# Optimization experiments

Measured on AMD Instinct MI355X. Metric: run time of the kernel, lower is better.

## Reference

```python
import jax, jax.numpy as jnp
import numpy as np


def setup_inputs() -> dict:
    key = jax.random.key(0)
    ks = jax.random.split(key, 10)
    B, C, T, H, W = 8, 128, 8, 32, 32
    Cq = C // 8
    return {
        "x": jax.random.normal(ks[0], (B, C, T, H, W), dtype=jnp.float32),
        "Wq": jax.random.normal(ks[1], (Cq, C), dtype=jnp.float32) * (1.0 / np.sqrt(C)),
        "bq": jax.random.normal(ks[2], (Cq,), dtype=jnp.float32) * 0.02,
        "Wk": jax.random.normal(ks[3], (Cq, C), dtype=jnp.float32) * (1.0 / np.sqrt(C)),
        "bk": jax.random.normal(ks[4], (Cq,), dtype=jnp.float32) * 0.02,
        "Wv": jax.random.normal(ks[5], (C, C), dtype=jnp.float32) * (1.0 / np.sqrt(C)),
        "bv": jax.random.normal(ks[6], (C,), dtype=jnp.float32) * 0.02,
        "gamma_pam": jax.random.normal(ks[7], (1,), dtype=jnp.float32),
        "gamma_cam": jax.random.normal(ks[8], (1,), dtype=jnp.float32),
        "gamma_tim": jax.random.normal(ks[9], (1,), dtype=jnp.float32),
    }


def reference(x, Wq, bq, Wk, bk, Wv, bv, gamma_pam, gamma_cam, gamma_tim):
    B, C, T, H, W = x.shape
    HW = H * W

    # ---- PAM: position attention over HW, feature dim = (C//8)*T ----
    # 1x1x1 Conv3d == per-position channel matmul
    q = jnp.einsum('bcthw,oc->bothw', x, Wq) + bq[None, :, None, None, None]
    k = jnp.einsum('bcthw,oc->bothw', x, Wk) + bk[None, :, None, None, None]
    v = jnp.einsum('bcthw,oc->bothw', x, Wv) + bv[None, :, None, None, None]
    qf = q.reshape(B, -1, HW)   # [B, (C//8)*T, HW]
    kf = k.reshape(B, -1, HW)
    vf = v.reshape(B, -1, HW)   # [B, C*T, HW]
    energy = jnp.einsum('bcn,bcm->bnm', qf, kf)          # [B, HW, HW]
    attn = jax.nn.softmax(energy, axis=-1)
    # out = bmm(v, attn^T)
    pam = jnp.einsum('bcm,bnm->bcn', vf, attn).reshape(B, C, T, H, W)
    pam = gamma_pam * pam + x

    # ---- CAM: channel attention (C x C) with negated-energy softmax ----
    xc = x.reshape(B, C, -1)                              # [B, C, T*HW]
    e = jnp.einsum('bcn,bdn->bcd', xc, xc)                # [B, C, C]
    e = jnp.max(e, axis=-1, keepdims=True) - e
    a = jax.nn.softmax(e, axis=-1)
    cam = jnp.einsum('bcd,bdn->bcn', a, xc).reshape(B, C, T, H, W)
    cam = gamma_cam * cam + x

    # ---- TIM: temporal attention (T x T) with negated-energy softmax ----
    xt = jnp.transpose(x, (0, 2, 1, 3, 4)).reshape(B, T, -1)  # [B, T, C*HW]
    e = jnp.einsum('btn,bsn->bts', xt, xt)                # [B, T, T]
    e = jnp.max(e, axis=-1, keepdims=True) - e
    a = jax.nn.softmax(e, axis=-1)
    tim = jnp.einsum('bts,bsn->btn', a, xt).reshape(B, T, C, H, W)
    tim = jnp.transpose(tim, (0, 2, 1, 3, 4))
    tim = gamma_tim * tim + x

    return pam + cam + tim
```

## Files before the change

kernel.cpp:

```cpp
#include <hip/hip_runtime.h>
#include <cstdint>

typedef unsigned short u16;
typedef __attribute__((ext_vector_type(8))) short bf16x8;
typedef __attribute__((ext_vector_type(4))) float f32x4;

constexpr int B_  = 8;
constexpr int C_  = 128;
constexpr int CQ  = 16;
constexpr int T_  = 8;
constexpr int HW_ = 1024;
constexpr int P_  = T_ * HW_;
constexpr int F_  = CQ * T_;
constexpr int CT_ = C_ * T_;

static __device__ __forceinline__ u16 f2bf(float f) {
    union { float f; unsigned u; } v; v.f = f;
    unsigned r = v.u + 0x7fffu + ((v.u >> 16) & 1u);
    return (u16)(r >> 16);
}

#define GLOAD16(src, dst)                                                     \
    __builtin_amdgcn_global_load_lds(                                         \
        (const __attribute__((address_space(1))) void*)(src),                 \
        (__attribute__((address_space(3))) void*)(dst), 16, 0, 0)

__global__ __launch_bounds__(256)
void k_qkv(const float* __restrict__ x,
           const float* __restrict__ Wq, const float* __restrict__ bq,
           const float* __restrict__ Wk, const float* __restrict__ bk,
           const float* __restrict__ Wv, const float* __restrict__ bv,
           u16* __restrict__ qt, u16* __restrict__ kt, u16* __restrict__ v16)
{
    __shared__ float xs[128][64];
    const int b   = blockIdx.y;
    const int p0  = blockIdx.x * 64;
    const int t   = p0 >> 10;
    const int hw0 = p0 & 1023;
    const int tid = threadIdx.x;

    #pragma unroll
    for (int r = 0; r < 8; r++) {
        int idx = r * 256 + tid;
        int c   = idx >> 4;
        int pj  = (idx & 15) << 2;
        *(float4*)&xs[c][pj] =
            *(const float4*)&x[((size_t)(b * C_ + c)) * P_ + p0 + pj];
    }
    __syncthreads();

    const int pq = (tid & 15) << 2;
    const int g  = tid >> 4;

    const float* wrow[10];
    float4       acc[10];
    #pragma unroll
    for (int j = 0; j < 10; j++) {
        int oc = g * 10 + j;
        float bias;
        if (oc < 16)      { wrow[j] = Wq + oc * C_;        bias = bq[oc]; }
        else if (oc < 32) { wrow[j] = Wk + (oc - 16) * C_; bias = bk[oc - 16]; }
        else              { wrow[j] = Wv + (oc - 32) * C_; bias = bv[oc - 32]; }
        acc[j] = make_float4(bias, bias, bias, bias);
    }

    for (int c4 = 0; c4 < 32; c4++) {
        float4 xv0 = *(float4*)&xs[c4 * 4 + 0][pq];
        float4 xv1 = *(float4*)&xs[c4 * 4 + 1][pq];
        float4 xv2 = *(float4*)&xs[c4 * 4 + 2][pq];
        float4 xv3 = *(float4*)&xs[c4 * 4 + 3][pq];
        #pragma unroll
        for (int j = 0; j < 10; j++) {
            float4 w = *(const float4*)&wrow[j][c4 * 4];
            acc[j].x += w.x * xv0.x + w.y * xv1.x + w.z * xv2.x + w.w * xv3.x;
            acc[j].y += w.x * xv0.y + w.y * xv1.y + w.z * xv2.y + w.w * xv3.y;
            acc[j].z += w.x * xv0.z + w.y * xv1.z + w.z * xv2.z + w.w * xv3.z;
            acc[j].w += w.x * xv0.w + w.y * xv1.w + w.z * xv2.w + w.w * xv3.w;
        }
    }

    #pragma unroll
    for (int j = 0; j < 10; j++) {
        int oc = g * 10 + j;
        float a4[4] = {acc[j].x, acc[j].y, acc[j].z, acc[j].w};
        if (oc < 16) {
            #pragma unroll
            for (int i = 0; i < 4; i++)
                qt[((size_t)b * HW_ + hw0 + pq + i) * F_ + oc * 8 + t] = f2bf(a4[i]);
        } else if (oc < 32) {
            #pragma unroll
            for (int i = 0; i < 4; i++)
                kt[((size_t)b * HW_ + hw0 + pq + i) * F_ + (oc - 16) * 8 + t] = f2bf(a4[i]);
        } else {
            ushort4 pk;
            pk.x = f2bf(a4[0]); pk.y = f2bf(a4[1]);
            pk.z = f2bf(a4[2]); pk.w = f2bf(a4[3]);
            *(ushort4*)&v16[((size_t)(b * C_ + oc - 32)) * P_ + p0 + pq] = pk;
        }
    }
}

__global__ __launch_bounds__(256)
void k_energy(const u16* __restrict__ qt, const u16* __restrict__ kt,
              float* __restrict__ E)
{
    __shared__ char As[32768];
    __shared__ char Bs[32768];
    const int b  = blockIdx.z;
    const int n0 = blockIdx.y * 128, m0 = blockIdx.x * 128;
    const int tid = threadIdx.x, lane = tid & 63, w = tid >> 6;
    const u16* qb = qt + (size_t)b * HW_ * F_;
    const u16* kb = kt + (size_t)b * HW_ * F_;

    #pragma unroll
    for (int i = 0; i < 8; i++) {
        int c    = w * 8 + i;
        int row  = c * 4 + (lane >> 4);
        int col  = ((lane & 15) ^ (row & 7)) * 8;
        GLOAD16(qb + (size_t)(n0 + row) * F_ + col, As + c * 1024);
        GLOAD16(kb + (size_t)(m0 + row) * F_ + col, Bs + c * 1024);
    }
    __syncthreads();

    const int wr = w >> 1, wc = w & 1;
    f32x4 acc[4][4];
    #pragma unroll
    for (int mi = 0; mi < 4; mi++)
        #pragma unroll
        for (int ni = 0; ni < 4; ni++) acc[mi][ni] = (f32x4){0.f, 0.f, 0.f, 0.f};

    #pragma unroll
    for (int ks = 0; ks < 4; ks++) {
        bf16x8 af[4], bg[4];
        #pragma unroll
        for (int mi = 0; mi < 4; mi++) {
            int row  = wr * 64 + mi * 16 + (lane & 15);
            int slot = (ks * 4 + (lane >> 4)) ^ (row & 7);
            af[mi] = *(const bf16x8*)(As + row * 256 + slot * 16);
            int rb  = wc * 64 + mi * 16 + (lane & 15);
            int sb  = (ks * 4 + (lane >> 4)) ^ (rb & 7);
            bg[mi] = *(const bf16x8*)(Bs + rb * 256 + sb * 16);
        }
        #pragma unroll
        for (int mi = 0; mi < 4; mi++)
            #pragma unroll
            for (int ni = 0; ni < 4; ni++)
                acc[mi][ni] = __builtin_amdgcn_mfma_f32_16x16x32_bf16(
                    af[mi], bg[ni], acc[mi][ni], 0, 0, 0);
    }

    float* Eb = E + (size_t)b * HW_ * HW_;
    #pragma unroll
    for (int mi = 0; mi < 4; mi++)
        #pragma unroll
        for (int ni = 0; ni < 4; ni++)
            #pragma unroll
            for (int r = 0; r < 4; r++)
                Eb[(size_t)(n0 + wr * 64 + mi * 16 + (lane >> 4) * 4 + r) * HW_
                   + m0 + wc * 64 + ni * 16 + (lane & 15)] = acc[mi][ni][r];
}

__global__ __launch_bounds__(256)
void k_softmax(const float* __restrict__ E, u16* __restrict__ A16)
{
    const float* e = E + (size_t)blockIdx.x * HW_;
    const int tid = threadIdx.x;
    float4 v = ((const float4*)e)[tid];
    float m = fmaxf(fmaxf(v.x, v.y), fmaxf(v.z, v.w));
    #pragma unroll
    for (int off = 32; off; off >>= 1) m = fmaxf(m, __shfl_xor(m, off));
    __shared__ float s1[4], s2[4];
    if ((tid & 63) == 0) s1[tid >> 6] = m;
    __syncthreads();
    m = fmaxf(fmaxf(s1[0], s1[1]), fmaxf(s1[2], s1[3]));
    v.x = __expf(v.x - m); v.y = __expf(v.y - m);
    v.z = __expf(v.z - m); v.w = __expf(v.w - m);
    float s = v.x + v.y + v.z + v.w;
    #pragma unroll
    for (int off = 32; off; off >>= 1) s += __shfl_xor(s, off);
    if ((tid & 63) == 0) s2[tid >> 6] = s;
    __syncthreads();
    s = s2[0] + s2[1] + s2[2] + s2[3];
    float inv = 1.0f / s;
    ushort4 pk;
    pk.x = f2bf(v.x * inv); pk.y = f2bf(v.y * inv);
    pk.z = f2bf(v.z * inv); pk.w = f2bf(v.w * inv);
    ((ushort4*)(A16 + (size_t)blockIdx.x * HW_))[tid] = pk;
}

__global__ __launch_bounds__(256)
void k_pv(const u16* __restrict__ v16, const u16* __restrict__ A16,
          const float* __restrict__ gamma_pam, float* __restrict__ out)
{
    __shared__ char As[16384];
    __shared__ char Bs[16384];
    const int b   = blockIdx.z;
    const int ct0 = blockIdx.y * 128, n0 = blockIdx.x * 128;
    const int tid = threadIdx.x, lane = tid & 63, w = tid >> 6;
    const u16* vb = v16 + (size_t)b * CT_ * HW_;
    const u16* ab = A16 + (size_t)b * HW_ * HW_;

    const int wr = w >> 1, wc = w & 1;
    f32x4 acc[4][4];
    #pragma unroll
    for (int mi = 0; mi < 4; mi++)
        #pragma unroll
        for (int ni = 0; ni < 4; ni++) acc[mi][ni] = (f32x4){0.f, 0.f, 0.f, 0.f};

    for (int mc = 0; mc < 1024; mc += 64) {
        #pragma unroll
        for (int i = 0; i < 4; i++) {
            int c   = w * 4 + i;
            int row = c * 8 + (lane >> 3);
            int col = ((lane & 7) ^ (row & 7)) * 8;
            GLOAD16(vb + (size_t)(ct0 + row) * HW_ + mc + col, As + c * 1024);
            GLOAD16(ab + (size_t)(n0  + row) * HW_ + mc + col, Bs + c * 1024);
        }
        __syncthreads();
        #pragma unroll
        for (int ks = 0; ks < 2; ks++) {
            bf16x8 af[4], bg[4];
            #pragma unroll
            for (int mi = 0; mi < 4; mi++) {
                int row  = wr * 64 + mi * 16 + (lane & 15);
                int slot = (ks * 4 + (lane >> 4)) ^ (row & 7);
                af[mi] = *(const bf16x8*)(As + row * 128 + slot * 16);
                int rb  = wc * 64 + mi * 16 + (lane & 15);
                int sb  = (ks * 4 + (lane >> 4)) ^ (rb & 7);
                bg[mi] = *(const bf16x8*)(Bs + rb * 128 + sb * 16);
            }
            #pragma unroll
            for (int mi = 0; mi < 4; mi++)
                #pragma unroll
                for (int ni = 0; ni < 4; ni++)
                    acc[mi][ni] = __builtin_amdgcn_mfma_f32_16x16x32_bf16(
                        af[mi], bg[ni], acc[mi][ni], 0, 0, 0);
        }
        __syncthreads();
    }

    const float gp = gamma_pam[0];
    float* ob = out + (size_t)b * CT_ * HW_;
    #pragma unroll
    for (int mi = 0; mi < 4; mi++)
        #pragma unroll
        for (int ni = 0; ni < 4; ni++)
            #pragma unroll
            for (int r = 0; r < 4; r++)
                ob[(size_t)(ct0 + wr * 64 + mi * 16 + (lane >> 4) * 4 + r) * HW_
                   + n0 + wc * 64 + ni * 16 + (lane & 15)] = gp * acc[mi][ni][r];
}

__global__ __launch_bounds__(256)
void k_cam_partial(const float* __restrict__ x, float* __restrict__ part)
{
    __shared__ float xs[64][132];
    const int b = blockIdx.y, ch = blockIdx.x;
    const int tid = threadIdx.x;
    const int n0 = ch * 256;
    const float* xb = x + (size_t)b * C_ * P_;
    const int tc = (tid & 15) << 3, td = (tid >> 4) << 3;
    float acc[8][8] = {};

    for (int sp = 0; sp < 4; sp++) {
        #pragma unroll
        for (int r = 0; r < 8; r++) {
            int idx = r * 256 + tid;
            int c = idx >> 4, nj = (idx & 15) << 2;
            float4 xv = *(const float4*)&xb[(size_t)c * P_ + n0 + sp * 64 + nj];
            xs[nj + 0][c] = xv.x; xs[nj + 1][c] = xv.y;
            xs[nj + 2][c] = xv.z; xs[nj + 3][c] = xv.w;
        }
        __syncthreads();
        for (int n = 0; n < 64; n++) {
            float4 a0 = *(float4*)&xs[n][tc], a1 = *(float4*)&xs[n][tc + 4];
            float4 b0 = *(float4*)&xs[n][td], b1 = *(float4*)&xs[n][td + 4];
            float av[8] = {a0.x, a0.y, a0.z, a0.w, a1.x, a1.y, a1.z, a1.w};
            float bv[8] = {b0.x, b0.y, b0.z, b0.w, b1.x, b1.y, b1.z, b1.w};
            #pragma unroll
            for (int i = 0; i < 8; i++)
                #pragma unroll
                for (int j = 0; j < 8; j++)
                    acc[i][j] += av[i] * bv[j];
        }
        __syncthreads();
    }
    float* pb = part + ((size_t)(b * 32 + ch)) * C_ * C_;
    #pragma unroll
    for (int i = 0; i < 8; i++) {
        *(float4*)&pb[(size_t)(tc + i) * C_ + td] =
            make_float4(acc[i][0], acc[i][1], acc[i][2], acc[i][3]);
        *(float4*)&pb[(size_t)(tc + i) * C_ + td + 4] =
            make_float4(acc[i][4], acc[i][5], acc[i][6], acc[i][7]);
    }
}

__global__ __launch_bounds__(128)
void k_cam_reduce(const float* __restrict__ part,
                  const float* __restrict__ gamma_cam, u16* __restrict__ acam16)
{
    const int b = blockIdx.y, c = blockIdx.x;
    const int d = threadIdx.x;
    float s = 0.f;
    for (int ch = 0; ch < 32; ch++)
        s += part[(((size_t)(b * 32 + ch)) * C_ + c) * C_ + d];
    float mn = s;
    #pragma unroll
    for (int off = 32; off; off >>= 1) mn = fminf(mn, __shfl_xor(mn, off));
    __shared__ float m1[2], m2[2];
    if ((d & 63) == 0) m1[d >> 6] = mn;
    __syncthreads();
    mn = fminf(m1[0], m1[1]);
    float p = __expf(mn - s);
    float sum = p;
    #pragma unroll
    for (int off = 32; off; off >>= 1) sum += __shfl_xor(sum, off);
    if ((d & 63) == 0) m2[d >> 6] = sum;
    __syncthreads();
    sum = m2[0] + m2[1];
    acam16[((size_t)(b * C_ + c)) * C_ + d] = f2bf(gamma_cam[0] * p / sum);
}

__global__ __launch_bounds__(256)
void k_tim_gram(const float* __restrict__ x, float* __restrict__ e_t)
{
    const int b = blockIdx.y, c = blockIdx.x;
    const int tid = threadIdx.x;
    const float* xb = x + ((size_t)(b * C_ + c)) * P_;
    float acc[8][8] = {};
    for (int r = 0; r < 4; r++) {
        int hw = r * 256 + tid;
        float xv[8];
        #pragma unroll
        for (int t = 0; t < 8; t++) xv[t] = xb[t * HW_ + hw];
        #pragma unroll
        for (int t = 0; t < 8; t++)
            #pragma unroll
            for (int s2 = 0; s2 < 8; s2++)
                acc[t][s2] += xv[t] * xv[s2];
    }
    __shared__ float sm[4][64];
    const int lane = tid & 63, wid = tid >> 6;
    #pragma unroll
    for (int u = 0; u < 64; u++) {
        float vv = acc[u >> 3][u & 7];
        #pragma unroll
        for (int off = 32; off; off >>= 1) vv += __shfl_xor(vv, off);
        if (lane == 0) sm[wid][u] = vv;
    }
    __syncthreads();
    if (tid < 64) {
        float vv = sm[0][tid] + sm[1][tid] + sm[2][tid] + sm[3][tid];
        atomicAdd(&e_t[b * 64 + tid], vv);
    }
}

__global__ __launch_bounds__(512)
void k_tim_softmax(const float* __restrict__ e_t, float* __restrict__ a_t)
{
    const int tid = threadIdx.x;
    float v = e_t[tid];
    float mn = v;
    #pragma unroll
    for (int off = 4; off; off >>= 1) mn = fminf(mn, __shfl_xor(mn, off, 8));
    float p = __expf(mn - v);
    float s = p;
    #pragma unroll
    for (int off = 4; off; off >>= 1) s += __shfl_xor(s, off, 8);
    a_t[tid] = p / s;
}

__global__ __launch_bounds__(256)
void k_xprime(const float* __restrict__ x, const float* __restrict__ atim,
              const float* __restrict__ gamma_tim, float* __restrict__ Xp)
{
    const int b = blockIdx.y, c = blockIdx.x;
    const size_t base = ((size_t)(b * C_ + c)) * P_;
    const int tid = threadIdx.x;
    const float gt = gamma_tim[0];

    float4 xv[8];
    #pragma unroll
    for (int t = 0; t < 8; t++)
        xv[t] = *(const float4*)&x[base + t * HW_ + tid * 4];

    #pragma unroll
    for (int t = 0; t < 8; t++) {
        float4 o = make_float4(3.f * xv[t].x, 3.f * xv[t].y,
                               3.f * xv[t].z, 3.f * xv[t].w);
        #pragma unroll
        for (int s = 0; s < 8; s++) {
            float w = gt * atim[b * 64 + t * 8 + s];
            o.x += w * xv[s].x; o.y += w * xv[s].y;
            o.z += w * xv[s].z; o.w += w * xv[s].w;
        }
        *(float4*)&Xp[base + t * HW_ + tid * 4] = o;
    }
}

__global__ __launch_bounds__(256)
void k_xt(const float* __restrict__ x, u16* __restrict__ xT)
{
    __shared__ char sy[32768];
    const int b  = blockIdx.y;
    const int p0 = blockIdx.x * 128;
    const int tid = threadIdx.x;

    #pragma unroll
    for (int r = 0; r < 16; r++) {
        int lin = r * 256 + tid;
        int c = lin >> 5, j4 = (lin & 31) << 2;
        float4 xv = *(const float4*)&x[((size_t)(b * C_ + c)) * P_ + p0 + j4];
        float a4[4] = {xv.x, xv.y, xv.z, xv.w};
        #pragma unroll
        for (int u = 0; u < 4; u++) {
            int pi = j4 + u;
            int byte = pi * 256 + ((c * 2) ^ (((pi >> 2) & 15) << 4));
            *(u16*)(sy + byte) = f2bf(a4[u]);
        }
    }
    __syncthreads();
    #pragma unroll
    for (int r = 0; r < 8; r++) {
        int lin = r * 256 + tid;
        int pi = lin >> 4, ci8 = (lin & 15) << 3;
        bf16x8 v = *(const bf16x8*)(sy + pi * 256 +
                                    ((ci8 * 2) ^ (((pi >> 2) & 15) << 4)));
        *(bf16x8*)&xT[((size_t)(b * P_ + p0 + pi)) * C_ + ci8] = v;
    }
}

__global__ __launch_bounds__(256)
void k_cam_av(const u16* __restrict__ acam16, const u16* __restrict__ xT,
              const float* __restrict__ Xp, float* __restrict__ out)
{
    const int b  = blockIdx.y;
    const int p0 = blockIdx.x * 128;
    const int tid = threadIdx.x, lane = tid & 63, w = tid >> 6;

    const u16* Ab = acam16 + (size_t)b * C_ * C_;
    const u16* Bb = xT + ((size_t)(b * P_ + p0 + w * 32)) * C_;

    f32x4 acc[8][2];
    #pragma unroll
    for (int mi = 0; mi < 8; mi++) {
        acc[mi][0] = (f32x4){0.f, 0.f, 0.f, 0.f};
        acc[mi][1] = (f32x4){0.f, 0.f, 0.f, 0.f};
    }

    bf16x8 bg[4][2];
    #pragma unroll
    for (int ks = 0; ks < 4; ks++)
        #pragma unroll
        for (int ni = 0; ni < 2; ni++)
            bg[ks][ni] = *(const bf16x8*)(Bb +
                (size_t)(ni * 16 + (lane & 15)) * C_ + ks * 32 + (lane >> 4) * 8);

    #pragma unroll
    for (int mi = 0; mi < 8; mi++) {
        #pragma unroll
        for (int ks = 0; ks < 4; ks++) {
            bf16x8 af = *(const bf16x8*)(Ab +
                (size_t)(mi * 16 + (lane & 15)) * C_ + ks * 32 + (lane >> 4) * 8);
            acc[mi][0] = __builtin_amdgcn_mfma_f32_16x16x32_bf16(
                af, bg[ks][0], acc[mi][0], 0, 0, 0);
            acc[mi][1] = __builtin_amdgcn_mfma_f32_16x16x32_bf16(
                af, bg[ks][1], acc[mi][1], 0, 0, 0);
        }
    }

    float* ob = out + (size_t)b * C_ * P_;
    const float* xp = Xp + (size_t)b * C_ * P_;
    #pragma unroll
    for (int mi = 0; mi < 8; mi++)
        #pragma unroll
        for (int ni = 0; ni < 2; ni++)
            #pragma unroll
            for (int r = 0; r < 4; r++) {
                int c = mi * 16 + (lane >> 4) * 4 + r;
                int p = p0 + w * 32 + ni * 16 + (lane & 15);
                size_t i = (size_t)c * P_ + p;
                ob[i] += acc[mi][ni][r] + xp[i];
            }
}

extern "C" void kernel_launch(void* const* d_in, const int* in_sizes, int n_in,
                              void* d_out, int out_size, void* d_ws, size_t ws_size,
                              hipStream_t stream)
{
    (void)in_sizes; (void)n_in; (void)out_size; (void)ws_size;
    const float* x  = (const float*)d_in[0];
    const float* Wq = (const float*)d_in[1];
    const float* bq = (const float*)d_in[2];
    const float* Wk = (const float*)d_in[3];
    const float* bk = (const float*)d_in[4];
    const float* Wv = (const float*)d_in[5];
    const float* bv = (const float*)d_in[6];
    const float* gp = (const float*)d_in[7];
    const float* gc = (const float*)d_in[8];
    const float* gt = (const float*)d_in[9];
    float* out = (float*)d_out;
    char*  ws  = (char*)d_ws;

    u16*   qtb    = (u16*)(ws + 0);
    u16*   ktb    = (u16*)(ws + (2u << 20));
    u16*   v16    = (u16*)(ws + (4u << 20));
    float* part   = (float*)(ws + (4u << 20));
    float* Ebuf   = (float*)(ws + (20u << 20));
    float* Xp     = (float*)(ws + (20u << 20));
    u16*   A16    = (u16*)(ws + (52u << 20));
    u16*   xT     = (u16*)(ws + (52u << 20));
    u16*   acam16 = (u16*)(ws + (68u << 20));
    float* etim   = (float*)(ws + (68u << 20) + 32768);
    float* atim   = etim + 512;

    hipMemsetAsync(etim, 0, 512 * sizeof(float), stream);

    k_qkv        <<<dim3(128, 8),  256, 0, stream>>>(x, Wq, bq, Wk, bk, Wv, bv,
                                                     qtb, ktb, v16);
    k_energy     <<<dim3(8, 8, 8), 256, 0, stream>>>(qtb, ktb, Ebuf);
    k_softmax    <<<dim3(8192),    256, 0, stream>>>(Ebuf, A16);
    k_tim_gram   <<<dim3(128, 8),  256, 0, stream>>>(x, etim);
    k_tim_softmax<<<dim3(1),       512, 0, stream>>>(etim, atim);
    k_pv         <<<dim3(8, 8, 8), 256, 0, stream>>>(v16, A16, gp, out);
    k_xprime     <<<dim3(128, 8),  256, 0, stream>>>(x, atim, gt, Xp);
    k_xt         <<<dim3(64, 8),   256, 0, stream>>>(x, xT);
    k_cam_partial<<<dim3(32, 8),   256, 0, stream>>>(x, part);
    k_cam_reduce <<<dim3(128, 8),  128, 0, stream>>>(part, gc, acam16);
    k_cam_av     <<<dim3(64, 8),   256, 0, stream>>>(acam16, xT, Xp, out);
}
```

Baseline: 322.6 us.

## Move QKV projection and CAM gram onto bf16 MFMA, store Xp in bf16

The QKV 1x1 conv now runs on MFMA. It takes a bf16 transposed copy of x produced up front by k_prep (which replaces k_xt) and bf16-cast weights from a new cast kernel. The CAM gram matrix, formerly an fp32 FMA outer-product kernel, is computed with a split bf16 hi/lo scheme (three MFMAs per tile) to keep near-fp32 accuracy. The temporal-mixed Xp intermediate is stored as bf16 to halve its traffic. These changes add extra kernels and split buffers that cost memory traffic, and they lower the precision of the projections and of Xp.

```diff
diff --git a/kernel.cpp b/kernel.cpp
--- a/kernel.cpp
+++ b/kernel.cpp
@@ -7,11 +7,10 @@
 
 constexpr int B_  = 8;
 constexpr int C_  = 128;
-constexpr int CQ  = 16;
 constexpr int T_  = 8;
 constexpr int HW_ = 1024;
 constexpr int P_  = T_ * HW_;
-constexpr int F_  = CQ * T_;
+constexpr int F_  = 128;
 constexpr int CT_ = C_ * T_;
 
 static __device__ __forceinline__ u16 f2bf(float f) {
@@ -19,6 +18,10 @@
     unsigned r = v.u + 0x7fffu + ((v.u >> 16) & 1u);
     return (u16)(r >> 16);
 }
+static __device__ __forceinline__ float bf2f(u16 h) {
+    union { unsigned u; float f; } v; v.u = ((unsigned)h) << 16;
+    return v.f;
+}
 
 #define GLOAD16(src, dst)                                                     \
     __builtin_amdgcn_global_load_lds(                                         \
@@ -26,78 +29,128 @@
         (__attribute__((address_space(3))) void*)(dst), 16, 0, 0)
 
 __global__ __launch_bounds__(256)
-void k_qkv(const float* __restrict__ x,
-           const float* __restrict__ Wq, const float* __restrict__ bq,
-           const float* __restrict__ Wk, const float* __restrict__ bk,
-           const float* __restrict__ Wv, const float* __restrict__ bv,
+void k_wcast(const float* __restrict__ Wq, const float* __restrict__ bq,
+             const float* __restrict__ Wk, const float* __restrict__ bk,
+             const float* __restrict__ Wv, const float* __restrict__ bv,
+             u16* __restrict__ Wall, float* __restrict__ ball)
+{
+    int tid = blockIdx.x * 256 + threadIdx.x;
+    if (tid < 20480) {
+        int oc = tid >> 7, c = tid & 127;
+        float w;
+        if (oc < 16)      w = Wq[oc * 128 + c];
+        else if (oc < 32) w = Wk[(oc - 16) * 128 + c];
+        else              w = Wv[(oc - 32) * 128 + c];
+        Wall[tid] = f2bf(w);
+    }
+    if (tid < 160) {
+        float bb;
+        if (tid < 16)      bb = bq[tid];
+        else if (tid < 32) bb = bk[tid - 16];
+        else               bb = bv[tid - 32];
+        ball[tid] = bb;
+    }
+}
+
+__global__ __launch_bounds__(256)
+void k_prep(const float* __restrict__ x, u16* __restrict__ xT)
+{
+    __shared__ char sy[32768];
+    const int b  = blockIdx.y;
+    const int p0 = blockIdx.x * 128;
+    const int tid = threadIdx.x;
+
+    #pragma unroll
+    for (int r = 0; r < 16; r++) {
+        int lin = r * 256 + tid;
+        int c = lin >> 5, j4 = (lin & 31) << 2;
+        float4 xv = *(const float4*)&x[((size_t)(b * C_ + c)) * P_ + p0 + j4];
+        float a4[4] = {xv.x, xv.y, xv.z, xv.w};
+        #pragma unroll
+        for (int u = 0; u < 4; u++) {
+            int pi = j4 + u;
+            int byte = pi * 256 + ((c * 2) ^ (((pi >> 2) & 15) << 4));
+            *(u16*)(sy + byte) = f2bf(a4[u]);
+        }
+    }
+    __syncthreads();
+    #pragma unroll
+    for (int r = 0; r < 8; r++) {
+        int lin = r * 256 + tid;
+        int pi = lin >> 4, ci8 = (lin & 15) << 3;
+        bf16x8 v = *(const bf16x8*)(sy + pi * 256 +
+                                    ((ci8 * 2) ^ (((pi >> 2) & 15) << 4)));
+        *(bf16x8*)&xT[((size_t)(b * P_ + p0 + pi)) * C_ + ci8] = v;
+    }
+}
+
+__global__ __launch_bounds__(256)
+void k_qkv(const u16* __restrict__ xT, const u16* __restrict__ Wall,
+           const float* __restrict__ ball,
            u16* __restrict__ qt, u16* __restrict__ kt, u16* __restrict__ v16)
 {
-    __shared__ float xs[128][64];
-    const int b   = blockIdx.y;
-    const int p0  = blockIdx.x * 64;
-    const int t   = p0 >> 10;
-    const int hw0 = p0 & 1023;
-    const int tid = threadIdx.x;
-
-    #pragma unroll
-    for (int r = 0; r < 8; r++) {
-        int idx = r * 256 + tid;
-        int c   = idx >> 4;
-        int pj  = (idx & 15) << 2;
-        *(float4*)&xs[c][pj] =
-            *(const float4*)&x[((size_t)(b * C_ + c)) * P_ + p0 + pj];
-    }
-    __syncthreads();
-
-    const int pq = (tid & 15) << 2;
-    const int g  = tid >> 4;
-
-    const float* wrow[10];
-    float4       acc[10];
-    #pragma unroll
-    for (int j = 0; j < 10; j++) {
-        int oc = g * 10 + j;
-        float bias;
-        if (oc < 16)      { wrow[j] = Wq + oc * C_;        bias = bq[oc]; }
-        else if (oc < 32) { wrow[j] = Wk + (oc - 16) * C_; bias = bk[oc - 16]; }
-        else              { wrow[j] = Wv + (oc - 32) * C_; bias = bv[oc - 32]; }
-        acc[j] = make_float4(bias, bias, bias, bias);
-    }
-
-    for (int c4 = 0; c4 < 32; c4++) {
-        float4 xv0 = *(float4*)&xs[c4 * 4 + 0][pq];
-        float4 xv1 = *(float4*)&xs[c4 * 4 + 1][pq];
-        float4 xv2 = *(float4*)&xs[c4 * 4 + 2][pq];
-        float4 xv3 = *(float4*)&xs[c4 * 4 + 3][pq];
-        #pragma unroll
-        for (int j = 0; j < 10; j++) {
-            float4 w = *(const float4*)&wrow[j][c4 * 4];
-            acc[j].x += w.x * xv0.x + w.y * xv1.x + w.z * xv2.x + w.w * xv3.x;
-            acc[j].y += w.x * xv0.y + w.y * xv1.y + w.z * xv2.y + w.w * xv3.y;
-            acc[j].z += w.x * xv0.z + w.y * xv1.z + w.z * xv2.z + w.w * xv3.z;
-            acc[j].w += w.x * xv0.w + w.y * xv1.w + w.z * xv2.w + w.w * xv3.w;
-        }
-    }
-
-    #pragma unroll
-    for (int j = 0; j < 10; j++) {
-        int oc = g * 10 + j;
-        float a4[4] = {acc[j].x, acc[j].y, acc[j].z, acc[j].w};
-        if (oc < 16) {
-            #pragma unroll
-            for (int i = 0; i < 4; i++)
-                qt[((size_t)b * HW_ + hw0 + pq + i) * F_ + oc * 8 + t] = f2bf(a4[i]);
-        } else if (oc < 32) {
-            #pragma unroll
-            for (int i = 0; i < 4; i++)
-                kt[((size_t)b * HW_ + hw0 + pq + i) * F_ + (oc - 16) * 8 + t] = f2bf(a4[i]);
-        } else {
-            ushort4 pk;
-            pk.x = f2bf(a4[0]); pk.y = f2bf(a4[1]);
-            pk.z = f2bf(a4[2]); pk.w = f2bf(a4[3]);
-            *(ushort4*)&v16[((size_t)(b * C_ + oc - 32)) * P_ + p0 + pq] = pk;
-        }
-    }
+    __shared__ char Ws[40960];
+    const int b  = blockIdx.y;
+    const int p0 = blockIdx.x * 128;
+    const int tid = threadIdx.x, lane = tid & 63, w = tid >> 6;
+
+    #pragma unroll
+    for (int i = 0; i < 10; i++) {
+        int ch  = w * 10 + i;
+        int row = ch * 4 + (lane >> 4);
+        int col = ((lane & 15) ^ (row & 7)) * 8;
+        GLOAD16(Wall + row * 128 + col, Ws + ch * 1024);
+    }
+
+    const u16* Bb = xT + ((size_t)(b * P_ + p0 + w * 32)) * F_;
+    bf16x8 bg[4][2];
+    #pragma unroll
+    for (int ks = 0; ks < 4; ks++)
+        #pragma unroll
+        for (int ni = 0; ni < 2; ni++)
+            bg[ks][ni] = *(const bf16x8*)(Bb +
+                (size_t)(ni * 16 + (lane & 15)) * F_ + ks * 32 + (lane >> 4) * 8);
+    __syncthreads();
+
+    f32x4 acc[10][2];
+    #pragma unroll
+    for (int mi = 0; mi < 10; mi++) {
+        acc[mi][0] = (f32x4){0.f, 0.f, 0.f, 0.f};
+        acc[mi][1] = (f32x4){0.f, 0.f, 0.f, 0.f};
+    }
+
+    #pragma unroll
+    for (int mi = 0; mi < 10; mi++) {
+        #pragma unroll
+        for (int ks = 0; ks < 4; ks++) {
+            int row  = mi * 16 + (lane & 15);
+            int slot = (ks * 4 + (lane >> 4)) ^ (row & 7);
+            bf16x8 af = *(const bf16x8*)(Ws + row * 256 + slot * 16);
+            acc[mi][0] = __builtin_amdgcn_mfma_f32_16x16x32_bf16(
+                af, bg[ks][0], acc[mi][0], 0, 0, 0);
+            acc[mi][1] = __builtin_amdgcn_mfma_f32_16x16x32_bf16(
+                af, bg[ks][1], acc[mi][1], 0, 0, 0);
+        }
+    }
+
+    const int t      = p0 >> 10;
+    const int hwbase = (p0 & 1023) + w * 32;
+    #pragma unroll
+    for (int mi = 0; mi < 10; mi++)
+        #pragma unroll
+        for (int ni = 0; ni < 2; ni++)
+            #pragma unroll
+            for (int r = 0; r < 4; r++) {
+                int oc = mi * 16 + (lane >> 4) * 4 + r;
+                int hw = hwbase + ni * 16 + (lane & 15);
+                u16 bv16 = f2bf(acc[mi][ni][r] + ball[oc]);
+                if (mi == 0)
+                    qt[((size_t)b * HW_ + hw) * F_ + oc * 8 + t] = bv16;
+                else if (mi == 1)
+                    kt[((size_t)b * HW_ + hw) * F_ + (oc - 16) * 8 + t] = bv16;
+                else
+                    v16[((size_t)(b * C_ + oc - 32)) * P_ + t * HW_ + hw] = bv16;
+            }
 }
 
 __global__ __launch_bounds__(256)
@@ -252,47 +305,90 @@
 }
 
 __global__ __launch_bounds__(256)
-void k_cam_partial(const float* __restrict__ x, float* __restrict__ part)
-{
-    __shared__ float xs[64][132];
+void k_split(const float* __restrict__ x, u16* __restrict__ xhi,
+             u16* __restrict__ xlo)
+{
+    for (int i = blockIdx.x * 256 + threadIdx.x; i < 2097152; i += 2048 * 256) {
+        float4 v = ((const float4*)x)[i];
+        ushort4 h, l;
+        h.x = f2bf(v.x); h.y = f2bf(v.y); h.z = f2bf(v.z); h.w = f2bf(v.w);
+        l.x = f2bf(v.x - bf2f(h.x)); l.y = f2bf(v.y - bf2f(h.y));
+        l.z = f2bf(v.z - bf2f(h.z)); l.w = f2bf(v.w - bf2f(h.w));
+        ((ushort4*)xhi)[i] = h;
+        ((ushort4*)xlo)[i] = l;
+    }
+}
+
+__global__ __launch_bounds__(256)
+void k_cam_gram(const u16* __restrict__ xhi, const u16* __restrict__ xlo,
+                float* __restrict__ part)
+{
+    __shared__ char Sh[32768];
+    __shared__ char Sl[32768];
     const int b = blockIdx.y, ch = blockIdx.x;
-    const int tid = threadIdx.x;
-    const int n0 = ch * 256;
-    const float* xb = x + (size_t)b * C_ * P_;
-    const int tc = (tid & 15) << 3, td = (tid >> 4) << 3;
-    float acc[8][8] = {};
-
-    for (int sp = 0; sp < 4; sp++) {
-        #pragma unroll
-        for (int r = 0; r < 8; r++) {
-            int idx = r * 256 + tid;
-            int c = idx >> 4, nj = (idx & 15) << 2;
-            float4 xv = *(const float4*)&xb[(size_t)c * P_ + n0 + sp * 64 + nj];
-            xs[nj + 0][c] = xv.x; xs[nj + 1][c] = xv.y;
-            xs[nj + 2][c] = xv.z; xs[nj + 3][c] = xv.w;
+    const int tid = threadIdx.x, lane = tid & 63, w = tid >> 6;
+    const u16* hb = xhi + (size_t)b * C_ * P_;
+    const u16* lb = xlo + (size_t)b * C_ * P_;
+
+    f32x4 acc[8][2];
+    #pragma unroll
+    for (int mi = 0; mi < 8; mi++) {
+        acc[mi][0] = (f32x4){0.f, 0.f, 0.f, 0.f};
+        acc[mi][1] = (f32x4){0.f, 0.f, 0.f, 0.f};
+    }
+
+    for (int kc = 0; kc < 2; kc++) {
+        int n0 = ch * 256 + kc * 128;
+        #pragma unroll
+        for (int i = 0; i < 8; i++) {
+            int c4  = w * 8 + i;
+            int row = c4 * 4 + (lane >> 4);
+            int col = ((lane & 15) ^ (row & 7)) * 8;
+            GLOAD16(hb + (size_t)row * P_ + n0 + col, Sh + c4 * 1024);
+            GLOAD16(lb + (size_t)row * P_ + n0 + col, Sl + c4 * 1024);
         }
         __syncthreads();
-        for (int n = 0; n < 64; n++) {
-            float4 a0 = *(float4*)&xs[n][tc], a1 = *(float4*)&xs[n][tc + 4];
-            float4 b0 = *(float4*)&xs[n][td], b1 = *(float4*)&xs[n][td + 4];
-            float av[8] = {a0.x, a0.y, a0.z, a0.w, a1.x, a1.y, a1.z, a1.w};
-            float bv[8] = {b0.x, b0.y, b0.z, b0.w, b1.x, b1.y, b1.z, b1.w};
-            #pragma unroll
-            for (int i = 0; i < 8; i++)
+        #pragma unroll
+        for (int ks = 0; ks < 4; ks++) {
+            bf16x8 bh[2], bl[2];
+            #pragma unroll
+            for (int ni = 0; ni < 2; ni++) {
+                int rb = w * 32 + ni * 16 + (lane & 15);
+                int sb = (ks * 4 + (lane >> 4)) ^ (rb & 7);
+                bh[ni] = *(const bf16x8*)(Sh + rb * 256 + sb * 16);
+                bl[ni] = *(const bf16x8*)(Sl + rb * 256 + sb * 16);
+            }
+            #pragma unroll
+            for (int mi = 0; mi < 8; mi++) {
+                int ra = mi * 16 + (lane & 15);
+                int sa = (ks * 4 + (lane >> 4)) ^ (ra & 7);
+                bf16x8 ah = *(const bf16x8*)(Sh + ra * 256 + sa * 16);
+                bf16x8 al = *(const bf16x8*)(Sl + ra * 256 + sa * 16);
                 #pragma unroll
-                for (int j = 0; j < 8; j++)
-                    acc[i][j] += av[i] * bv[j];
+                for (int ni = 0; ni < 2; ni++) {
+                    acc[mi][ni] = __builtin_amdgcn_mfma_f32_16x16x32_bf16(
+                        ah, bh[ni], acc[mi][ni], 0, 0, 0);
+                    acc[mi][ni] = __builtin_amdgcn_mfma_f32_16x16x32_bf16(
+                        ah, bl[ni], acc[mi][ni], 0, 0, 0);
+                    acc[mi][ni] = __builtin_amdgcn_mfma_f32_16x16x32_bf16(
+                        al, bh[ni], acc[mi][ni], 0, 0, 0);
+                }
+            }
         }
         __syncthreads();
     }
-    float* pb = part + ((size_t)(b * 32 + ch)) * C_ * C_;
-    #pragma unroll
-    for (int i = 0; i < 8; i++) {
-        *(float4*)&pb[(size_t)(tc + i) * C_ + td] =
-            make_float4(acc[i][0], acc[i][1], acc[i][2], acc[i][3]);
-        *(float4*)&pb[(size_t)(tc + i) * C_ + td + 4] =
-            make_float4(acc[i][4], acc[i][5], acc[i][6], acc[i][7]);
-    }
+
+    float* pb = part + ((size_t)(b * 32 + ch)) * 16384;
+    #pragma unroll
+    for (int mi = 0; mi < 8; mi++)
+        #pragma unroll
+        for (int ni = 0; ni < 2; ni++)
+            #pragma unroll
+            for (int r = 0; r < 4; r++) {
+                int c = mi * 16 + (lane >> 4) * 4 + r;
+                int d = w * 32 + ni * 16 + (lane & 15);
+                pb[c * 128 + d] = acc[mi][ni][r];
+            }
 }
 
 __global__ __launch_bounds__(128)
@@ -372,7 +468,7 @@
 
 __global__ __launch_bounds__(256)
 void k_xprime(const float* __restrict__ x, const float* __restrict__ atim,
-              const float* __restrict__ gamma_tim, float* __restrict__ Xp)
+              const float* __restrict__ gamma_tim, u16* __restrict__ Xp)
 {
     const int b = blockIdx.y, c = blockIdx.x;
     const size_t base = ((size_t)(b * C_ + c)) * P_;
@@ -394,45 +490,15 @@
             o.x += w * xv[s].x; o.y += w * xv[s].y;
             o.z += w * xv[s].z; o.w += w * xv[s].w;
         }
-        *(float4*)&Xp[base + t * HW_ + tid * 4] = o;
-    }
-}
-
-__global__ __launch_bounds__(256)
-void k_xt(const float* __restrict__ x, u16* __restrict__ xT)
-{
-    __shared__ char sy[32768];
-    const int b  = blockIdx.y;
-    const int p0 = blockIdx.x * 128;
-    const int tid = threadIdx.x;
-
-    #pragma unroll
-    for (int r = 0; r < 16; r++) {
-        int lin = r * 256 + tid;
-        int c = lin >> 5, j4 = (lin & 31) << 2;
-        float4 xv = *(const float4*)&x[((size_t)(b * C_ + c)) * P_ + p0 + j4];
-        float a4[4] = {xv.x, xv.y, xv.z, xv.w};
-        #pragma unroll
-        for (int u = 0; u < 4; u++) {
-            int pi = j4 + u;
-            int byte = pi * 256 + ((c * 2) ^ (((pi >> 2) & 15) << 4));
-            *(u16*)(sy + byte) = f2bf(a4[u]);
-        }
-    }
-    __syncthreads();
-    #pragma unroll
-    for (int r = 0; r < 8; r++) {
-        int lin = r * 256 + tid;
-        int pi = lin >> 4, ci8 = (lin & 15) << 3;
-        bf16x8 v = *(const bf16x8*)(sy + pi * 256 +
-                                    ((ci8 * 2) ^ (((pi >> 2) & 15) << 4)));
-        *(bf16x8*)&xT[((size_t)(b * P_ + p0 + pi)) * C_ + ci8] = v;
+        ushort4 pk;
+        pk.x = f2bf(o.x); pk.y = f2bf(o.y); pk.z = f2bf(o.z); pk.w = f2bf(o.w);
+        *(ushort4*)&Xp[base + t * HW_ + tid * 4] = pk;
     }
 }
 
 __global__ __launch_bounds__(256)
 void k_cam_av(const u16* __restrict__ acam16, const u16* __restrict__ xT,
-              const float* __restrict__ Xp, float* __restrict__ out)
+              const u16* __restrict__ Xp, float* __restrict__ out)
 {
     const int b  = blockIdx.y;
     const int p0 = blockIdx.x * 128;
@@ -470,7 +536,7 @@
     }
 
     float* ob = out + (size_t)b * C_ * P_;
-    const float* xp = Xp + (size_t)b * C_ * P_;
+    const u16* xp = Xp + (size_t)b * C_ * P_;
     #pragma unroll
     for (int mi = 0; mi < 8; mi++)
         #pragma unroll
@@ -480,7 +546,7 @@
                 int c = mi * 16 + (lane >> 4) * 4 + r;
                 int p = p0 + w * 32 + ni * 16 + (lane & 15);
                 size_t i = (size_t)c * P_ + p;
-                ob[i] += acc[mi][ni][r] + xp[i];
+                ob[i] += acc[mi][ni][r] + bf2f(xp[i]);
             }
 }
 
@@ -502,30 +568,38 @@
     float* out = (float*)d_out;
     char*  ws  = (char*)d_ws;
 
-    u16*   qtb    = (u16*)(ws + 0);
-    u16*   ktb    = (u16*)(ws + (2u << 20));
-    u16*   v16    = (u16*)(ws + (4u << 20));
-    float* part   = (float*)(ws + (4u << 20));
-    float* Ebuf   = (float*)(ws + (20u << 20));
-    float* Xp     = (float*)(ws + (20u << 20));
-    u16*   A16    = (u16*)(ws + (52u << 20));
-    u16*   xT     = (u16*)(ws + (52u << 20));
-    u16*   acam16 = (u16*)(ws + (68u << 20));
-    float* etim   = (float*)(ws + (68u << 20) + 32768);
-    float* atim   = etim + 512;
+    const size_t MiB = 1u << 20;
+    u16*   xT     = (u16*)(ws + 0);
+    u16*   qtb    = (u16*)(ws + 16 * MiB);
+    u16*   ktb    = (u16*)(ws + 18 * MiB);
+    u16*   v16    = (u16*)(ws + 20 * MiB);
+    u16*   Xp16   = (u16*)(ws + 20 * MiB);
+    float* Ebuf   = (float*)(ws + 36 * MiB);
+    u16*   xhi    = (u16*)(ws + 36 * MiB);
+    u16*   xlo    = (u16*)(ws + 52 * MiB);
+    u16*   A16    = (u16*)(ws + 68 * MiB);
+    float* part   = (float*)(ws + 68 * MiB);
+    u16*   acam16 = (u16*)(ws + 84 * MiB);
+    u16*   Wall   = (u16*)(ws + 84 * MiB + 65536);
+    float* ball   = (float*)(ws + 84 * MiB + 131072);
+    float* etim   = (float*)(ws + 84 * MiB + 139264);
+    float* atim   = (float*)(ws + 84 * MiB + 143360);
 
     hipMemsetAsync(etim, 0, 512 * sizeof(float), stream);
 
-    k_qkv        <<<dim3(128, 8),  256, 0, stream>>>(x, Wq, bq, Wk, bk, Wv, bv,
+    k_wcast      <<<dim3(80),      256, 0, stream>>>(Wq, bq, Wk, bk, Wv, bv,
+                                                     Wall, ball);
+    k_prep       <<<dim3(64, 8),   256, 0, stream>>>(x, xT);
+    k_qkv        <<<dim3(64, 8),   256, 0, stream>>>(xT, Wall, ball,
                                                      qtb, ktb, v16);
     k_energy     <<<dim3(8, 8, 8), 256, 0, stream>>>(qtb, ktb, Ebuf);
     k_softmax    <<<dim3(8192),    256, 0, stream>>>(Ebuf, A16);
+    k_split      <<<dim3(2048),    256, 0, stream>>>(x, xhi, xlo);
     k_tim_gram   <<<dim3(128, 8),  256, 0, stream>>>(x, etim);
     k_tim_softmax<<<dim3(1),       512, 0, stream>>>(etim, atim);
     k_pv         <<<dim3(8, 8, 8), 256, 0, stream>>>(v16, A16, gp, out);
-    k_xprime     <<<dim3(128, 8),  256, 0, stream>>>(x, atim, gt, Xp);
-    k_xt         <<<dim3(64, 8),   256, 0, stream>>>(x, xT);
-    k_cam_partial<<<dim3(32, 8),   256, 0, stream>>>(x, part);
+    k_xprime     <<<dim3(128, 8),  256, 0, stream>>>(x, atim, gt, Xp16);
+    k_cam_gram   <<<dim3(32, 8),   256, 0, stream>>>(xhi, xlo, part);
     k_cam_reduce <<<dim3(128, 8),  128, 0, stream>>>(part, gc, acam16);
-    k_cam_av     <<<dim3(64, 8),   256, 0, stream>>>(acam16, xT, Xp, out);
-}
+    k_cam_av     <<<dim3(64, 8),   256, 0, stream>>>(acam16, xT, Xp16, out);
+}
```

Result: faster. 263.4 us (-18.4%).
